# Optimization experiments

Measured on AMD Instinct MI355X. Metric: run time of the kernel, lower is better.

Reference implementation:

```python
import jax, jax.numpy as jnp
import numpy as np

N = 50000      # nodes
E = 800000     # edges (avg degree 16)
D = 128        # node_embedding_dim
H = 256        # hidden_dim


def setup_inputs() -> dict:
    key = jax.random.key(0)
    ks = jax.random.split(key, 12)
    init = lambda k, shape, fan: (jax.random.normal(k, shape, jnp.float32) / np.sqrt(fan).astype(np.float32))
    return {
        "node_ids": jnp.arange(N, dtype=jnp.int32),
        "edge_index": jax.random.randint(ks[0], (2, E), 0, N, jnp.int32),
        "neighbour_edge_index": jax.random.randint(ks[1], (2, E), 0, N, jnp.int32),
        "edge_attr": jax.random.uniform(ks[2], (E,), jnp.float32),
        "emb": init(ks[3], (N, D), D),          # Embedding table
        "W_in": init(ks[4], (D, H), D), "b_in": jnp.zeros((H,), jnp.float32),
        "W_out": init(ks[5], (H, D), H), "b_out": jnp.zeros((D,), jnp.float32),
        "W1": init(ks[6], (2 * D, D), 2 * D), "b1": jnp.zeros((D,), jnp.float32),
        "W2": init(ks[7], (D, D), D), "b2": jnp.zeros((D,), jnp.float32),
        "W3": init(ks[8], (D, 1), D), "b3": jnp.zeros((1,), jnp.float32),
    }


def gcn_conv(x, W, b, edge_index, w):
    """PyG GCNConv, add_self_loops=False, normalize=True.
    out_i = b + sum_{(j->i)} d_i^{-1/2} w_ji d_j^{-1/2} (x_j @ W)
    deg_i = sum of incoming edge weights at target node i.
    """
    row, col = edge_index[0], edge_index[1]
    deg = jax.ops.segment_sum(w, col, num_segments=N)
    dinv = jnp.where(deg > 0, 1.0 / jnp.sqrt(deg), 0.0)
    norm = dinv[row] * w * dinv[col]                    # [E]
    h = x @ W                                           # [N, out]
    msg = h[row] * norm[:, None]                        # [E, out]
    return jax.ops.segment_sum(msg, col, num_segments=N) + b


def reference(node_ids, edge_index, neighbour_edge_index, edge_attr,
              emb, W_in, b_in, W_out, b_out, W1, b1, W2, b2, W3, b3):
    x = emb[node_ids]                                   # embedding lookup [N, D]
    x = jax.nn.elu(gcn_conv(x, W_in, b_in, edge_index, edge_attr))
    ones = jnp.ones((neighbour_edge_index.shape[1],), x.dtype)
    x = jax.nn.elu(gcn_conv(x, W_out, b_out, neighbour_edge_index, ones))
    # edge-level gather-concat-MLP decoder
    src, dst = edge_index[0], edge_index[1]
    h = jnp.concatenate([x[src], x[dst]], axis=1)       # [E, 2D]
    h = jax.nn.relu(h @ W1 + b1)
    h = jax.nn.relu(h @ W2 + b2)
    return (h @ W3 + b3).squeeze(-1)                    # [E]
```

## Files before the change

### kernel.cpp

```cpp
#include <hip/hip_runtime.h>
#include <math.h>

#define NN 50000
#define NE 800000

typedef __attribute__((ext_vector_type(8))) short s8_t;
typedef __attribute__((ext_vector_type(4))) float f4_t;

__device__ __forceinline__ short bf16_rne(float v) {
  unsigned u = __float_as_uint(v);
  unsigned r = (u + 0x7FFFu + ((u >> 16) & 1u)) >> 16;
  return (short)r;
}
__device__ __forceinline__ float bf16_tof(short h) {
  return __uint_as_float(((unsigned)(unsigned short)h) << 16);
}
__device__ __forceinline__ void split2(float v, short& hi, short& lo) {
  hi = bf16_rne(v);
  lo = bf16_rne(v - bf16_tof(hi));
}


__global__ __launch_bounds__(256) void k_wcvt(const float* __restrict__ W1,
                                              const float* __restrict__ W2,
                                              const float* __restrict__ W_in,
                                              const float* __restrict__ W_out,
                                              short* __restrict__ w1th,
                                              short* __restrict__ w1tl,
                                              short* __restrict__ w2th,
                                              short* __restrict__ w2tl,
                                              short* __restrict__ winth,
                                              short* __restrict__ wintl,
                                              short* __restrict__ woutth,
                                              short* __restrict__ wouttl) {
  int i = blockIdx.x * 256 + threadIdx.x;
  if (i < 32768) {
    int k = i >> 7, n = i & 127;
    short h, l; split2(W1[i], h, l);
    w1th[n * 256 + k] = h; w1tl[n * 256 + k] = l;
  } else if (i < 49152) {
    int j = i - 32768;
    int k = j >> 7, n = j & 127;
    short h, l; split2(W2[j], h, l);
    w2th[n * 128 + k] = h; w2tl[n * 128 + k] = l;
  } else if (i < 81920) {
    int j = i - 49152;
    int k = j >> 8, n = j & 255;
    short h, l; split2(W_in[j], h, l);
    winth[n * 128 + k] = h; wintl[n * 128 + k] = l;
  } else if (i < 114688) {
    int j = i - 81920;
    int k = j >> 7, n = j & 127;
    short h, l; split2(W_out[j], h, l);
    woutth[n * 256 + k] = h; wouttl[n * 256 + k] = l;
  }
}


__global__ __launch_bounds__(256) void k_hist(const int* __restrict__ ei,
                                              const int* __restrict__ nei,
                                              const float* __restrict__ w,
                                              int* __restrict__ cnt1,
                                              float* __restrict__ deg1,
                                              int* __restrict__ cnt2) {
  int e = blockIdx.x * 256 + threadIdx.x;
  if (e < NE) {
    int c1 = ei[NE + e];
    atomicAdd(&cnt1[c1], 1);
    atomicAdd(&deg1[c1], w[e]);
    atomicAdd(&cnt2[nei[NE + e]], 1);
  }
}

__global__ __launch_bounds__(256) void k_dinvs(const float* __restrict__ deg1,
                                               const int* __restrict__ cnt2,
                                               float* __restrict__ dinv1,
                                               float* __restrict__ dinv2) {
  int i = blockIdx.x * 256 + threadIdx.x;
  if (i < NN) {
    float d1 = deg1[i];
    dinv1[i] = d1 > 0.f ? (1.0f / sqrtf(d1)) : 0.f;
    int c2 = cnt2[i];
    dinv2[i] = c2 > 0 ? (1.0f / sqrtf((float)c2)) : 0.f;
  }
}


#define NCHUNK 196

__global__ __launch_bounds__(256) void k_scan_part(const int* __restrict__ cnt1,
                                                   const int* __restrict__ cnt2,
                                                   int* __restrict__ part) {
  int g = blockIdx.x >= NCHUNK;
  int chunk = g ? blockIdx.x - NCHUNK : blockIdx.x;
  const int* cnt = g ? cnt2 : cnt1;
  int i = chunk * 256 + threadIdx.x;
  int v = (i < NN) ? cnt[i] : 0;
  __shared__ int sd[4];
#pragma unroll
  for (int o = 32; o; o >>= 1) v += __shfl_down(v, o);
  if ((threadIdx.x & 63) == 0) sd[threadIdx.x >> 6] = v;
  __syncthreads();
  if (threadIdx.x == 0) part[blockIdx.x] = sd[0] + sd[1] + sd[2] + sd[3];
}

__global__ __launch_bounds__(256) void k_scan_mid(int* __restrict__ part,
                                                  int* __restrict__ off1_last,
                                                  int* __restrict__ off2_last) {
  __shared__ int sd[256];
  for (int g = 0; g < 2; g++) {
    int base = g * NCHUNK;
    int v = (threadIdx.x < NCHUNK) ? part[base + threadIdx.x] : 0;
    sd[threadIdx.x] = v;
    __syncthreads();
    for (int o = 1; o < 256; o <<= 1) {
      int x = (threadIdx.x >= o) ? sd[threadIdx.x - o] : 0;
      __syncthreads();
      sd[threadIdx.x] += x;
      __syncthreads();
    }
    if (threadIdx.x < NCHUNK) part[base + threadIdx.x] = sd[threadIdx.x] - v;
    if (threadIdx.x == 255) *(g ? off2_last : off1_last) = sd[255];
    __syncthreads();
  }
}

__global__ __launch_bounds__(256) void k_scan_final(const int* __restrict__ cnt1,
                                                    const int* __restrict__ cnt2,
                                                    const int* __restrict__ part,
                                                    int* __restrict__ off1,
                                                    int* __restrict__ pos1,
                                                    int* __restrict__ off2,
                                                    int* __restrict__ pos2) {
  int g = blockIdx.x >= NCHUNK;
  int chunk = g ? blockIdx.x - NCHUNK : blockIdx.x;
  const int* cnt = g ? cnt2 : cnt1;
  int* off = g ? off2 : off1;
  int* pos = g ? pos2 : pos1;
  __shared__ int sd[256];
  int i = chunk * 256 + threadIdx.x;
  int v = (i < NN) ? cnt[i] : 0;
  sd[threadIdx.x] = v;
  __syncthreads();
  for (int o = 1; o < 256; o <<= 1) {
    int x = (threadIdx.x >= o) ? sd[threadIdx.x - o] : 0;
    __syncthreads();
    sd[threadIdx.x] += x;
    __syncthreads();
  }
  if (i < NN) {
    int ex = part[blockIdx.x] + sd[threadIdx.x] - v;
    off[i] = ex; pos[i] = ex;
  }
}


__global__ __launch_bounds__(256) void k_fill(const int* __restrict__ ei,
                                              const int* __restrict__ nei,
                                              const float* __restrict__ w,
                                              const float* __restrict__ dinv1,
                                              const float* __restrict__ dinv2,
                                              int* __restrict__ pos1,
                                              int4* __restrict__ c1pack,
                                              int* __restrict__ pos2,
                                              int2* __restrict__ c2pack) {
  int e = blockIdx.x * 256 + threadIdx.x;
  if (e < NE) {
    int r = ei[e], c = ei[NE + e];
    float nv = dinv1[r] * w[e] * dinv1[c];
    int s = atomicAdd(&pos1[c], 1);
    c1pack[s] = make_int4(r, c, e, __float_as_int(nv));
    int r2 = nei[e], c2v = nei[NE + e];
    float nv2 = dinv2[r2] * dinv2[c2v];
    int s2 = atomicAdd(&pos2[c2v], 1);
    c2pack[s2] = make_int2(r2, __float_as_int(nv2));
  }
}


__global__ __launch_bounds__(256) void k_agg1(const int* __restrict__ off,
                                              const int4* __restrict__ c1pack,
                                              const int* __restrict__ ids,
                                              const float* __restrict__ emb,
                                              short* __restrict__ aggXh,
                                              short* __restrict__ aggXl) {
  int wave = threadIdx.x >> 6, lane = threadIdx.x & 63;
  int h = lane >> 5, sub = lane & 31;
  int node = blockIdx.x * 4 + wave;
  int start = off[node], end = off[node + 1];
  float4 acc = make_float4(0.f, 0.f, 0.f, 0.f);
  int i = start + h;
  for (; i + 14 < end; i += 16) {
    float4 v[8]; float n[8];
#pragma unroll
    for (int k = 0; k < 8; k++) {
      int4 p = c1pack[i + 2 * k];
      n[k] = __int_as_float(p.w);
      v[k] = *(const float4*)(emb + (size_t)ids[p.x] * 128 + sub * 4);
    }
#pragma unroll
    for (int k = 0; k < 8; k++) {
      acc.x = fmaf(n[k], v[k].x, acc.x);
      acc.y = fmaf(n[k], v[k].y, acc.y);
      acc.z = fmaf(n[k], v[k].z, acc.z);
      acc.w = fmaf(n[k], v[k].w, acc.w);
    }
  }
  for (; i < end; i += 2) {
    int4 p = c1pack[i];
    float n0 = __int_as_float(p.w);
    float4 v0 = *(const float4*)(emb + (size_t)ids[p.x] * 128 + sub * 4);
    acc.x = fmaf(n0, v0.x, acc.x);
    acc.y = fmaf(n0, v0.y, acc.y);
    acc.z = fmaf(n0, v0.z, acc.z);
    acc.w = fmaf(n0, v0.w, acc.w);
  }
  acc.x += __shfl_xor(acc.x, 32);
  acc.y += __shfl_xor(acc.y, 32);
  acc.z += __shfl_xor(acc.z, 32);
  acc.w += __shfl_xor(acc.w, 32);
  if (h == 0) {
    short h0, l0, h1, l1, h2, l2, h3, l3;
    split2(acc.x, h0, l0); split2(acc.y, h1, l1);
    split2(acc.z, h2, l2); split2(acc.w, h3, l3);
    uint2 hp, lp;
    hp.x = (unsigned)(unsigned short)h0 | ((unsigned)(unsigned short)h1 << 16);
    hp.y = (unsigned)(unsigned short)h2 | ((unsigned)(unsigned short)h3 << 16);
    lp.x = (unsigned)(unsigned short)l0 | ((unsigned)(unsigned short)l1 << 16);
    lp.y = (unsigned)(unsigned short)l2 | ((unsigned)(unsigned short)l3 << 16);
    *(uint2*)(aggXh + (size_t)node * 128 + sub * 4) = hp;
    *(uint2*)(aggXl + (size_t)node * 128 + sub * 4) = lp;
  }
}


__global__ __launch_bounds__(256) void k_agg2(const int* __restrict__ off,
                                              const int2* __restrict__ c2pack,
                                              const float* __restrict__ h2,
                                              const float* __restrict__ b,
                                              short* __restrict__ xh,
                                              short* __restrict__ xl) {
  int wave = threadIdx.x >> 6, lane = threadIdx.x & 63;
  int h = lane >> 5, sub = lane & 31;
  int node = blockIdx.x * 4 + wave;
  int start = off[node], end = off[node + 1];
  float4 acc = make_float4(0.f, 0.f, 0.f, 0.f);
  int i = start + h;
  for (; i + 14 < end; i += 16) {
    float4 v[8]; float n[8];
#pragma unroll
    for (int k = 0; k < 8; k++) {
      int2 p = c2pack[i + 2 * k];
      n[k] = __int_as_float(p.y);
      v[k] = *(const float4*)(h2 + (size_t)p.x * 128 + sub * 4);
    }
#pragma unroll
    for (int k = 0; k < 8; k++) {
      acc.x = fmaf(n[k], v[k].x, acc.x);
      acc.y = fmaf(n[k], v[k].y, acc.y);
      acc.z = fmaf(n[k], v[k].z, acc.z);
      acc.w = fmaf(n[k], v[k].w, acc.w);
    }
  }
  for (; i < end; i += 2) {
    int2 p = c2pack[i];
    float n0 = __int_as_float(p.y);
    float4 v0 = *(const float4*)(h2 + (size_t)p.x * 128 + sub * 4);
    acc.x = fmaf(n0, v0.x, acc.x);
    acc.y = fmaf(n0, v0.y, acc.y);
    acc.z = fmaf(n0, v0.z, acc.z);
    acc.w = fmaf(n0, v0.w, acc.w);
  }
  acc.x += __shfl_xor(acc.x, 32);
  acc.y += __shfl_xor(acc.y, 32);
  acc.z += __shfl_xor(acc.z, 32);
  acc.w += __shfl_xor(acc.w, 32);
  if (h == 0) {
    float4 bb = *(const float4*)(b + sub * 4);
    float v0 = acc.x + bb.x, v1 = acc.y + bb.y;
    float v2 = acc.z + bb.z, v3 = acc.w + bb.w;
    v0 = v0 > 0.f ? v0 : expm1f(v0);
    v1 = v1 > 0.f ? v1 : expm1f(v1);
    v2 = v2 > 0.f ? v2 : expm1f(v2);
    v3 = v3 > 0.f ? v3 : expm1f(v3);
    short h0, l0, h1, l1, h2s, l2, h3, l3;
    split2(v0, h0, l0); split2(v1, h1, l1);
    split2(v2, h2s, l2); split2(v3, h3, l3);
    uint2 hp, lp;
    hp.x = (unsigned)(unsigned short)h0 | ((unsigned)(unsigned short)h1 << 16);
    hp.y = (unsigned)(unsigned short)h2s | ((unsigned)(unsigned short)h3 << 16);
    lp.x = (unsigned)(unsigned short)l0 | ((unsigned)(unsigned short)l1 << 16);
    lp.y = (unsigned)(unsigned short)l2 | ((unsigned)(unsigned short)l3 << 16);
    *(uint2*)(xh + (size_t)node * 128 + sub * 4) = hp;
    *(uint2*)(xl + (size_t)node * 128 + sub * 4) = lp;
  }
}


__global__ __launch_bounds__(256) void k_gemm1m(const short* __restrict__ aggXh,
                                                const short* __restrict__ aggXl,
                                                const short* __restrict__ winth,
                                                const short* __restrict__ wintl,
                                                const float* __restrict__ b,
                                                short* __restrict__ x1h,
                                                short* __restrict__ x1l) {
  __shared__ short Xh[32 * 136];
  __shared__ short Xl[32 * 136];
  int t = threadIdx.x;
  int n0 = blockIdx.x * 32;
#pragma unroll
  for (int j = 0; j < 2; j++) {
    int i = t + 256 * j;
    int row = i >> 4, q = i & 15;
    int node = n0 + row; if (node >= NN) node = NN - 1;
    *(uint4*)&Xh[row * 136 + q * 8] = *(const uint4*)(aggXh + (size_t)node * 128 + q * 8);
    *(uint4*)&Xl[row * 136 + q * 8] = *(const uint4*)(aggXl + (size_t)node * 128 + q * 8);
  }
  __syncthreads();

  int w = t >> 6, lane = t & 63;
  int quad = lane >> 4, l16 = lane & 15;
  int nb = w * 64;
  int aoff0 = l16 * 136 + quad * 8;
  int aoff1 = (16 + l16) * 136 + quad * 8;

  f4_t acc[2][4];
#pragma unroll
  for (int mi = 0; mi < 2; mi++)
#pragma unroll
    for (int ni = 0; ni < 4; ni++) acc[mi][ni] = (f4_t){0.f, 0.f, 0.f, 0.f};

#pragma unroll
  for (int kb = 0; kb < 4; kb++) {
    int k0 = kb * 32;
    s8_t ah0 = *(const s8_t*)&Xh[aoff0 + k0];
    s8_t ah1 = *(const s8_t*)&Xh[aoff1 + k0];
    s8_t al0 = *(const s8_t*)&Xl[aoff0 + k0];
    s8_t al1 = *(const s8_t*)&Xl[aoff1 + k0];
#pragma unroll
    for (int ni = 0; ni < 4; ni++) {
      int bo = (nb + ni * 16 + l16) * 128 + quad * 8 + k0;
      s8_t bh = *(const s8_t*)(winth + bo);
      s8_t bl = *(const s8_t*)(wintl + bo);
      acc[0][ni] = __builtin_amdgcn_mfma_f32_16x16x32_bf16(ah0, bh, acc[0][ni], 0, 0, 0);
      acc[0][ni] = __builtin_amdgcn_mfma_f32_16x16x32_bf16(ah0, bl, acc[0][ni], 0, 0, 0);
      acc[0][ni] = __builtin_amdgcn_mfma_f32_16x16x32_bf16(al0, bh, acc[0][ni], 0, 0, 0);
      acc[1][ni] = __builtin_amdgcn_mfma_f32_16x16x32_bf16(ah1, bh, acc[1][ni], 0, 0, 0);
      acc[1][ni] = __builtin_amdgcn_mfma_f32_16x16x32_bf16(ah1, bl, acc[1][ni], 0, 0, 0);
      acc[1][ni] = __builtin_amdgcn_mfma_f32_16x16x32_bf16(al1, bh, acc[1][ni], 0, 0, 0);
    }
  }

#pragma unroll
  for (int mi = 0; mi < 2; mi++)
#pragma unroll
    for (int ni = 0; ni < 4; ni++) {
      int col = nb + ni * 16 + l16;
      float bv = b[col];
#pragma unroll
      for (int r = 0; r < 4; r++) {
        int node = n0 + mi * 16 + quad * 4 + r;
        if (node < NN) {
          float v = acc[mi][ni][r] + bv;
          v = v > 0.f ? v : expm1f(v);
          short hh, ll; split2(v, hh, ll);
          x1h[(size_t)node * 256 + col] = hh;
          x1l[(size_t)node * 256 + col] = ll;
        }
      }
    }
}


__global__ __launch_bounds__(256) void k_gemm2m(const short* __restrict__ x1h,
                                                const short* __restrict__ x1l,
                                                const short* __restrict__ woutth,
                                                const short* __restrict__ wouttl,
                                                float* __restrict__ h2) {
  __shared__ short Xh[32 * 264];
  __shared__ short Xl[32 * 264];
  int t = threadIdx.x;
  int n0 = blockIdx.x * 32;
#pragma unroll
  for (int j = 0; j < 4; j++) {
    int i = t + 256 * j;
    int row = i >> 5, q = i & 31;
    int node = n0 + row; if (node >= NN) node = NN - 1;
    *(uint4*)&Xh[row * 264 + q * 8] = *(const uint4*)(x1h + (size_t)node * 256 + q * 8);
    *(uint4*)&Xl[row * 264 + q * 8] = *(const uint4*)(x1l + (size_t)node * 256 + q * 8);
  }
  __syncthreads();

  int w = t >> 6, lane = t & 63;
  int quad = lane >> 4, l16 = lane & 15;
  int nb = w * 32;
  int aoff0 = l16 * 264 + quad * 8;
  int aoff1 = (16 + l16) * 264 + quad * 8;

  f4_t acc[2][2];
#pragma unroll
  for (int mi = 0; mi < 2; mi++)
#pragma unroll
    for (int ni = 0; ni < 2; ni++) acc[mi][ni] = (f4_t){0.f, 0.f, 0.f, 0.f};

#pragma unroll
  for (int kb = 0; kb < 8; kb++) {
    int k0 = kb * 32;
    s8_t ah0 = *(const s8_t*)&Xh[aoff0 + k0];
    s8_t ah1 = *(const s8_t*)&Xh[aoff1 + k0];
    s8_t al0 = *(const s8_t*)&Xl[aoff0 + k0];
    s8_t al1 = *(const s8_t*)&Xl[aoff1 + k0];
#pragma unroll
    for (int ni = 0; ni < 2; ni++) {
      int bo = (nb + ni * 16 + l16) * 256 + quad * 8 + k0;
      s8_t bh = *(const s8_t*)(woutth + bo);
      s8_t bl = *(const s8_t*)(wouttl + bo);
      acc[0][ni] = __builtin_amdgcn_mfma_f32_16x16x32_bf16(ah0, bh, acc[0][ni], 0, 0, 0);
      acc[0][ni] = __builtin_amdgcn_mfma_f32_16x16x32_bf16(ah0, bl, acc[0][ni], 0, 0, 0);
      acc[0][ni] = __builtin_amdgcn_mfma_f32_16x16x32_bf16(al0, bh, acc[0][ni], 0, 0, 0);
      acc[1][ni] = __builtin_amdgcn_mfma_f32_16x16x32_bf16(ah1, bh, acc[1][ni], 0, 0, 0);
      acc[1][ni] = __builtin_amdgcn_mfma_f32_16x16x32_bf16(ah1, bl, acc[1][ni], 0, 0, 0);
      acc[1][ni] = __builtin_amdgcn_mfma_f32_16x16x32_bf16(al1, bh, acc[1][ni], 0, 0, 0);
    }
  }

#pragma unroll
  for (int mi = 0; mi < 2; mi++)
#pragma unroll
    for (int ni = 0; ni < 2; ni++) {
      int col = nb + ni * 16 + l16;
#pragma unroll
      for (int r = 0; r < 4; r++) {
        int node = n0 + mi * 16 + quad * 4 + r;
        if (node < NN) h2[(size_t)node * 128 + col] = acc[mi][ni][r];
      }
    }
}


__global__ __launch_bounds__(256) void k_pab(const short* __restrict__ x2h,
                                             const short* __restrict__ x2l,
                                             const short* __restrict__ w1th,
                                             const short* __restrict__ w1tl,
                                             const float* __restrict__ b1,
                                             float* __restrict__ Pa,
                                             float* __restrict__ Pb) {
  __shared__ short Xh[32 * 136];
  __shared__ short Xl[32 * 136];
  int t = threadIdx.x;
  int n0 = blockIdx.x * 32;
#pragma unroll
  for (int j = 0; j < 2; j++) {
    int i = t + 256 * j;
    int row = i >> 4, q = i & 15;
    int node = n0 + row; if (node >= NN) node = NN - 1;
    *(uint4*)&Xh[row * 136 + q * 8] = *(const uint4*)(x2h + (size_t)node * 128 + q * 8);
    *(uint4*)&Xl[row * 136 + q * 8] = *(const uint4*)(x2l + (size_t)node * 128 + q * 8);
  }
  __syncthreads();

  int w = t >> 6, lane = t & 63;
  int quad = lane >> 4, l16 = lane & 15;
  int nb = w * 32;
  int aoff0 = l16 * 136 + quad * 8;
  int aoff1 = (16 + l16) * 136 + quad * 8;
  int bo0 = (nb + l16) * 256 + quad * 8;
  int bo1 = (nb + 16 + l16) * 256 + quad * 8;

  f4_t aa[2][2], ab[2][2];
#pragma unroll
  for (int mi = 0; mi < 2; mi++)
#pragma unroll
    for (int ni = 0; ni < 2; ni++) {
      aa[mi][ni] = (f4_t){0.f, 0.f, 0.f, 0.f};
      ab[mi][ni] = (f4_t){0.f, 0.f, 0.f, 0.f};
    }

#pragma unroll
  for (int kb = 0; kb < 4; kb++) {
    int k0 = kb * 32;
    s8_t ah0 = *(const s8_t*)&Xh[aoff0 + k0];
    s8_t ah1 = *(const s8_t*)&Xh[aoff1 + k0];
    s8_t al0 = *(const s8_t*)&Xl[aoff0 + k0];
    s8_t al1 = *(const s8_t*)&Xl[aoff1 + k0];
    {
      s8_t bh0 = *(const s8_t*)(w1th + bo0 + k0);
      s8_t bh1 = *(const s8_t*)(w1th + bo1 + k0);
      s8_t bl0 = *(const s8_t*)(w1tl + bo0 + k0);
      s8_t bl1 = *(const s8_t*)(w1tl + bo1 + k0);
      aa[0][0] = __builtin_amdgcn_mfma_f32_16x16x32_bf16(ah0, bh0, aa[0][0], 0, 0, 0);
      aa[0][0] = __builtin_amdgcn_mfma_f32_16x16x32_bf16(ah0, bl0, aa[0][0], 0, 0, 0);
      aa[0][0] = __builtin_amdgcn_mfma_f32_16x16x32_bf16(al0, bh0, aa[0][0], 0, 0, 0);
      aa[0][1] = __builtin_amdgcn_mfma_f32_16x16x32_bf16(ah0, bh1, aa[0][1], 0, 0, 0);
      aa[0][1] = __builtin_amdgcn_mfma_f32_16x16x32_bf16(ah0, bl1, aa[0][1], 0, 0, 0);
      aa[0][1] = __builtin_amdgcn_mfma_f32_16x16x32_bf16(al0, bh1, aa[0][1], 0, 0, 0);
      aa[1][0] = __builtin_amdgcn_mfma_f32_16x16x32_bf16(ah1, bh0, aa[1][0], 0, 0, 0);
      aa[1][0] = __builtin_amdgcn_mfma_f32_16x16x32_bf16(ah1, bl0, aa[1][0], 0, 0, 0);
      aa[1][0] = __builtin_amdgcn_mfma_f32_16x16x32_bf16(al1, bh0, aa[1][0], 0, 0, 0);
      aa[1][1] = __builtin_amdgcn_mfma_f32_16x16x32_bf16(ah1, bh1, aa[1][1], 0, 0, 0);
      aa[1][1] = __builtin_amdgcn_mfma_f32_16x16x32_bf16(ah1, bl1, aa[1][1], 0, 0, 0);
      aa[1][1] = __builtin_amdgcn_mfma_f32_16x16x32_bf16(al1, bh1, aa[1][1], 0, 0, 0);
    }
    {
      s8_t bh0 = *(const s8_t*)(w1th + bo0 + 128 + k0);
      s8_t bh1 = *(const s8_t*)(w1th + bo1 + 128 + k0);
      s8_t bl0 = *(const s8_t*)(w1tl + bo0 + 128 + k0);
      s8_t bl1 = *(const s8_t*)(w1tl + bo1 + 128 + k0);
      ab[0][0] = __builtin_amdgcn_mfma_f32_16x16x32_bf16(ah0, bh0, ab[0][0], 0, 0, 0);
      ab[0][0] = __builtin_amdgcn_mfma_f32_16x16x32_bf16(ah0, bl0, ab[0][0], 0, 0, 0);
      ab[0][0] = __builtin_amdgcn_mfma_f32_16x16x32_bf16(al0, bh0, ab[0][0], 0, 0, 0);
      ab[0][1] = __builtin_amdgcn_mfma_f32_16x16x32_bf16(ah0, bh1, ab[0][1], 0, 0, 0);
      ab[0][1] = __builtin_amdgcn_mfma_f32_16x16x32_bf16(ah0, bl1, ab[0][1], 0, 0, 0);
      ab[0][1] = __builtin_amdgcn_mfma_f32_16x16x32_bf16(al0, bh1, ab[0][1], 0, 0, 0);
      ab[1][0] = __builtin_amdgcn_mfma_f32_16x16x32_bf16(ah1, bh0, ab[1][0], 0, 0, 0);
      ab[1][0] = __builtin_amdgcn_mfma_f32_16x16x32_bf16(ah1, bl0, ab[1][0], 0, 0, 0);
      ab[1][0] = __builtin_amdgcn_mfma_f32_16x16x32_bf16(al1, bh0, ab[1][0], 0, 0, 0);
      ab[1][1] = __builtin_amdgcn_mfma_f32_16x16x32_bf16(ah1, bh1, ab[1][1], 0, 0, 0);
      ab[1][1] = __builtin_amdgcn_mfma_f32_16x16x32_bf16(ah1, bl1, ab[1][1], 0, 0, 0);
      ab[1][1] = __builtin_amdgcn_mfma_f32_16x16x32_bf16(al1, bh1, ab[1][1], 0, 0, 0);
    }
  }

  float b1v0 = b1[nb + l16], b1v1 = b1[nb + 16 + l16];
#pragma unroll
  for (int mi = 0; mi < 2; mi++)
#pragma unroll
    for (int ni = 0; ni < 2; ni++) {
      int col = nb + ni * 16 + l16;
      float bv = ni ? b1v1 : b1v0;
#pragma unroll
      for (int r = 0; r < 4; r++) {
        int node = n0 + mi * 16 + quad * 4 + r;
        if (node < NN) {
          Pa[(size_t)node * 128 + col] = aa[mi][ni][r];
          Pb[(size_t)node * 128 + col] = ab[mi][ni][r] + bv;
        }
      }
    }
}


#define ST 136

__global__ __launch_bounds__(256, 4) void k_decoder(
    const float* __restrict__ Pa, const float* __restrict__ Pb,
    const int4* __restrict__ c1pack,
    const short* __restrict__ w2th, const short* __restrict__ w2tl,
    const float* __restrict__ b2,
    const float* __restrict__ W3, const float* __restrict__ b3,
    float* __restrict__ out) {
  __shared__ short Th[32 * ST];
  __shared__ short Tl[32 * ST];
  __shared__ float part[4][32];

  int t = threadIdx.x;
  int b = blockIdx.x;
  int id = (b & 7) * 3125 + (b >> 3);
  int s0base = id * 32;

#pragma unroll
  for (int j = 0; j < 2; j++) {
    int i = t + 256 * j;
    int le = i >> 4, q = i & 15;
    int4 p = c1pack[s0base + le];
    const float* pa = Pa + (size_t)p.x * 128 + q * 8;
    const float* pb = Pb + (size_t)p.y * 128 + q * 8;
    float4 a0 = *(const float4*)(pa);
    float4 a1 = *(const float4*)(pa + 4);
    float4 c0 = *(const float4*)(pb);
    float4 c1 = *(const float4*)(pb + 4);
    float v[8];
    v[0] = a0.x + c0.x; v[1] = a0.y + c0.y;
    v[2] = a0.z + c0.z; v[3] = a0.w + c0.w;
    v[4] = a1.x + c1.x; v[5] = a1.y + c1.y;
    v[6] = a1.z + c1.z; v[7] = a1.w + c1.w;
    s8_t hv, lv;
#pragma unroll
    for (int k = 0; k < 8; k++) {
      float x = fmaxf(v[k], 0.f);
      short h, l; split2(x, h, l);
      hv[k] = h; lv[k] = l;
    }
    *(s8_t*)&Th[le * ST + q * 8] = hv;
    *(s8_t*)&Tl[le * ST + q * 8] = lv;
  }
  __syncthreads();

  int w = t >> 6, lane = t & 63;
  int quad = lane >> 4, l16 = lane & 15;
  int nb = w * 32;
  float b2v0 = b2[nb + l16], b2v1 = b2[nb + 16 + l16];
  float w3a = W3[nb + l16], w3b = W3[nb + 16 + l16];

  int toff0 = l16 * ST + quad * 8;
  int toff1 = (16 + l16) * ST + quad * 8;
  int coff0 = (nb + l16) * 128 + quad * 8;
  int coff1 = (nb + 16 + l16) * 128 + quad * 8;

  f4_t acc2[2][2];
#pragma unroll
  for (int mi = 0; mi < 2; mi++)
#pragma unroll
    for (int ni = 0; ni < 2; ni++) acc2[mi][ni] = (f4_t){0.f, 0.f, 0.f, 0.f};

#pragma unroll
  for (int kb = 0; kb < 4; kb++) {
    int k0 = kb * 32;
    s8_t ah0 = *(const s8_t*)&Th[toff0 + k0];
    s8_t ah1 = *(const s8_t*)&Th[toff1 + k0];
    s8_t al0 = *(const s8_t*)&Tl[toff0 + k0];
    s8_t al1 = *(const s8_t*)&Tl[toff1 + k0];
    s8_t bh0 = *(const s8_t*)(w2th + coff0 + k0);
    s8_t bh1 = *(const s8_t*)(w2th + coff1 + k0);
    s8_t bl0 = *(const s8_t*)(w2tl + coff0 + k0);
    s8_t bl1 = *(const s8_t*)(w2tl + coff1 + k0);
    acc2[0][0] = __builtin_amdgcn_mfma_f32_16x16x32_bf16(ah0, bh0, acc2[0][0], 0, 0, 0);
    acc2[0][0] = __builtin_amdgcn_mfma_f32_16x16x32_bf16(ah0, bl0, acc2[0][0], 0, 0, 0);
    acc2[0][0] = __builtin_amdgcn_mfma_f32_16x16x32_bf16(al0, bh0, acc2[0][0], 0, 0, 0);
    acc2[0][1] = __builtin_amdgcn_mfma_f32_16x16x32_bf16(ah0, bh1, acc2[0][1], 0, 0, 0);
    acc2[0][1] = __builtin_amdgcn_mfma_f32_16x16x32_bf16(ah0, bl1, acc2[0][1], 0, 0, 0);
    acc2[0][1] = __builtin_amdgcn_mfma_f32_16x16x32_bf16(al0, bh1, acc2[0][1], 0, 0, 0);
    acc2[1][0] = __builtin_amdgcn_mfma_f32_16x16x32_bf16(ah1, bh0, acc2[1][0], 0, 0, 0);
    acc2[1][0] = __builtin_amdgcn_mfma_f32_16x16x32_bf16(ah1, bl0, acc2[1][0], 0, 0, 0);
    acc2[1][0] = __builtin_amdgcn_mfma_f32_16x16x32_bf16(al1, bh0, acc2[1][0], 0, 0, 0);
    acc2[1][1] = __builtin_amdgcn_mfma_f32_16x16x32_bf16(ah1, bh1, acc2[1][1], 0, 0, 0);
    acc2[1][1] = __builtin_amdgcn_mfma_f32_16x16x32_bf16(ah1, bl1, acc2[1][1], 0, 0, 0);
    acc2[1][1] = __builtin_amdgcn_mfma_f32_16x16x32_bf16(al1, bh1, acc2[1][1], 0, 0, 0);
  }

#pragma unroll
  for (int mi = 0; mi < 2; mi++) {
#pragma unroll
    for (int r = 0; r < 4; r++) {
      float pv = fmaxf(acc2[mi][0][r] + b2v0, 0.f) * w3a +
                 fmaxf(acc2[mi][1][r] + b2v1, 0.f) * w3b;
      pv += __shfl_xor(pv, 1);
      pv += __shfl_xor(pv, 2);
      pv += __shfl_xor(pv, 4);
      pv += __shfl_xor(pv, 8);
      if (l16 == 0) part[w][mi * 16 + quad * 4 + r] = pv;
    }
  }
  __syncthreads();

  if (t < 32) {
    float s = part[0][t] + part[1][t] + part[2][t] + part[3][t] + b3[0];
    int4 p = c1pack[s0base + t];
    out[p.z] = s;
  }
}


extern "C" void kernel_launch(void* const* d_in, const int* in_sizes, int n_in,
                              void* d_out, int out_size, void* d_ws, size_t ws_size,
                              hipStream_t stream) {
  const int*   node_ids = (const int*)d_in[0];
  const int*   ei       = (const int*)d_in[1];
  const int*   nei      = (const int*)d_in[2];
  const float* eattr    = (const float*)d_in[3];
  const float* emb      = (const float*)d_in[4];
  const float* W_in     = (const float*)d_in[5];
  const float* b_in     = (const float*)d_in[6];
  const float* W_out    = (const float*)d_in[7];
  const float* b_out    = (const float*)d_in[8];
  const float* W1       = (const float*)d_in[9];
  const float* b1       = (const float*)d_in[10];
  const float* W2       = (const float*)d_in[11];
  const float* b2       = (const float*)d_in[12];
  const float* W3       = (const float*)d_in[13];
  const float* b3       = (const float*)d_in[14];
  float* out = (float*)d_out;

  float* ws    = (float*)d_ws;
  float* bufA  = ws;
  float* bufB  = bufA + (size_t)NN * 128;
  int*   cnt1  = (int*)(bufB + (size_t)NN * 256);
  int*   cnt2  = cnt1 + NN;
  float* deg1  = (float*)(cnt2 + NN);
  float* dinv1 = deg1 + NN;
  float* dinv2 = dinv1 + NN;
  int*   off1  = (int*)(dinv2 + NN);
  int*   pos1  = off1 + NN + 1;
  int*   off2  = pos1 + NN;
  int*   pos2  = off2 + NN + 1;
  int4*  c1pack = (int4*)((((uintptr_t)(pos2 + NN)) + 15) & ~(uintptr_t)15);
  int2*  c2pack = (int2*)(c1pack + NE);
  short* w1th   = (short*)(c2pack + NE);
  short* w1tl   = w1th + 32768;
  short* w2th   = w1tl + 32768;
  short* w2tl   = w2th + 16384;
  short* winth  = w2tl + 16384;
  short* wintl  = winth + 32768;
  short* woutth = wintl + 32768;
  short* wouttl = woutth + 32768;
  int*   part   = (int*)(wouttl + 32768);

  short* aggXh = (short*)bufA;
  short* aggXl = aggXh + (size_t)NN * 128;
  float* h2    = bufA;
  float* Pa    = bufA;
  short* x1h   = (short*)bufB;
  short* x1l   = x1h + (size_t)NN * 256;
  short* x2h   = (short*)bufB;
  short* x2l   = x2h + (size_t)NN * 128;
  float* Pb    = bufB + (size_t)NN * 128;

  k_wcvt<<<448, 256, 0, stream>>>(W1, W2, W_in, W_out,
                                  w1th, w1tl, w2th, w2tl,
                                  winth, wintl, woutth, wouttl);

  hipMemsetAsync(cnt1, 0, 3 * (size_t)NN * sizeof(int), stream);
  k_hist<<<NE / 256, 256, 0, stream>>>(ei, nei, eattr, cnt1, deg1, cnt2);
  k_dinvs<<<(NN + 255) / 256, 256, 0, stream>>>(deg1, cnt2, dinv1, dinv2);
  k_scan_part<<<2 * NCHUNK, 256, 0, stream>>>(cnt1, cnt2, part);
  k_scan_mid<<<1, 256, 0, stream>>>(part, off1 + NN, off2 + NN);
  k_scan_final<<<2 * NCHUNK, 256, 0, stream>>>(cnt1, cnt2, part,
                                               off1, pos1, off2, pos2);
  k_fill<<<NE / 256, 256, 0, stream>>>(ei, nei, eattr, dinv1, dinv2,
                                       pos1, c1pack, pos2, c2pack);

  k_agg1<<<NN / 4, 256, 0, stream>>>(off1, c1pack, node_ids, emb, aggXh, aggXl);
  k_gemm1m<<<(NN + 31) / 32, 256, 0, stream>>>(aggXh, aggXl, winth, wintl,
                                               b_in, x1h, x1l);

  k_gemm2m<<<(NN + 31) / 32, 256, 0, stream>>>(x1h, x1l, woutth, wouttl, h2);
  k_agg2<<<NN / 4, 256, 0, stream>>>(off2, c2pack, h2, b_out, x2h, x2l);

  k_pab<<<(NN + 31) / 32, 256, 0, stream>>>(x2h, x2l, w1th, w1tl, b1, Pa, Pb);

  k_decoder<<<NE / 32, 256, 0, stream>>>(Pa, Pb, c1pack,
                                         w2th, w2tl, b2, W3, b3, out);
}
```

Baseline: 760.7 us.

## Fuse neighbour aggregation into following GEMM kernels and merge dinv into scan

After: 797.9 us. +4.9%, slower.

```diff
diff --git a/kernel.cpp b/kernel.cpp
--- a/kernel.cpp
+++ b/kernel.cpp
@@ -72,34 +72,33 @@
   }
 }
 
-__global__ __launch_bounds__(256) void k_dinvs(const float* __restrict__ deg1,
-                                               const int* __restrict__ cnt2,
-                                               float* __restrict__ dinv1,
-                                               float* __restrict__ dinv2) {
-  int i = blockIdx.x * 256 + threadIdx.x;
-  if (i < NN) {
-    float d1 = deg1[i];
-    dinv1[i] = d1 > 0.f ? (1.0f / sqrtf(d1)) : 0.f;
-    int c2 = cnt2[i];
-    dinv2[i] = c2 > 0 ? (1.0f / sqrtf((float)c2)) : 0.f;
-  }
-}
-
 
 #define NCHUNK 196
 
 __global__ __launch_bounds__(256) void k_scan_part(const int* __restrict__ cnt1,
                                                    const int* __restrict__ cnt2,
+                                                   const float* __restrict__ deg1,
+                                                   float* __restrict__ dinv1,
+                                                   float* __restrict__ dinv2,
                                                    int* __restrict__ part) {
   int g = blockIdx.x >= NCHUNK;
   int chunk = g ? blockIdx.x - NCHUNK : blockIdx.x;
   const int* cnt = g ? cnt2 : cnt1;
   int i = chunk * 256 + threadIdx.x;
   int v = (i < NN) ? cnt[i] : 0;
+  if (i < NN) {
+    if (!g) {
+      float d1 = deg1[i];
+      dinv1[i] = d1 > 0.f ? (1.0f / sqrtf(d1)) : 0.f;
+    } else {
+      dinv2[i] = v > 0 ? (1.0f / sqrtf((float)v)) : 0.f;
+    }
+  }
   __shared__ int sd[4];
-#pragma unroll
-  for (int o = 32; o; o >>= 1) v += __shfl_down(v, o);
-  if ((threadIdx.x & 63) == 0) sd[threadIdx.x >> 6] = v;
+  int r = v;
+#pragma unroll
+  for (int o = 32; o; o >>= 1) r += __shfl_down(r, o);
+  if ((threadIdx.x & 63) == 0) sd[threadIdx.x >> 6] = r;
   __syncthreads();
   if (threadIdx.x == 0) part[blockIdx.x] = sd[0] + sd[1] + sd[2] + sd[3];
 }
@@ -178,147 +177,77 @@
 }
 
 
-__global__ __launch_bounds__(256) void k_agg1(const int* __restrict__ off,
-                                              const int4* __restrict__ c1pack,
-                                              const int* __restrict__ ids,
-                                              const float* __restrict__ emb,
-                                              short* __restrict__ aggXh,
-                                              short* __restrict__ aggXl) {
-  int wave = threadIdx.x >> 6, lane = threadIdx.x & 63;
-  int h = lane >> 5, sub = lane & 31;
-  int node = blockIdx.x * 4 + wave;
-  int start = off[node], end = off[node + 1];
-  float4 acc = make_float4(0.f, 0.f, 0.f, 0.f);
-  int i = start + h;
-  for (; i + 14 < end; i += 16) {
-    float4 v[8]; float n[8];
-#pragma unroll
-    for (int k = 0; k < 8; k++) {
-      int4 p = c1pack[i + 2 * k];
-      n[k] = __int_as_float(p.w);
-      v[k] = *(const float4*)(emb + (size_t)ids[p.x] * 128 + sub * 4);
-    }
-#pragma unroll
-    for (int k = 0; k < 8; k++) {
-      acc.x = fmaf(n[k], v[k].x, acc.x);
-      acc.y = fmaf(n[k], v[k].y, acc.y);
-      acc.z = fmaf(n[k], v[k].z, acc.z);
-      acc.w = fmaf(n[k], v[k].w, acc.w);
-    }
-  }
-  for (; i < end; i += 2) {
-    int4 p = c1pack[i];
-    float n0 = __int_as_float(p.w);
-    float4 v0 = *(const float4*)(emb + (size_t)ids[p.x] * 128 + sub * 4);
-    acc.x = fmaf(n0, v0.x, acc.x);
-    acc.y = fmaf(n0, v0.y, acc.y);
-    acc.z = fmaf(n0, v0.z, acc.z);
-    acc.w = fmaf(n0, v0.w, acc.w);
-  }
-  acc.x += __shfl_xor(acc.x, 32);
-  acc.y += __shfl_xor(acc.y, 32);
-  acc.z += __shfl_xor(acc.z, 32);
-  acc.w += __shfl_xor(acc.w, 32);
-  if (h == 0) {
-    short h0, l0, h1, l1, h2, l2, h3, l3;
-    split2(acc.x, h0, l0); split2(acc.y, h1, l1);
-    split2(acc.z, h2, l2); split2(acc.w, h3, l3);
-    uint2 hp, lp;
-    hp.x = (unsigned)(unsigned short)h0 | ((unsigned)(unsigned short)h1 << 16);
-    hp.y = (unsigned)(unsigned short)h2 | ((unsigned)(unsigned short)h3 << 16);
-    lp.x = (unsigned)(unsigned short)l0 | ((unsigned)(unsigned short)l1 << 16);
-    lp.y = (unsigned)(unsigned short)l2 | ((unsigned)(unsigned short)l3 << 16);
-    *(uint2*)(aggXh + (size_t)node * 128 + sub * 4) = hp;
-    *(uint2*)(aggXl + (size_t)node * 128 + sub * 4) = lp;
-  }
-}
-
-
-__global__ __launch_bounds__(256) void k_agg2(const int* __restrict__ off,
-                                              const int2* __restrict__ c2pack,
-                                              const float* __restrict__ h2,
-                                              const float* __restrict__ b,
-                                              short* __restrict__ xh,
-                                              short* __restrict__ xl) {
-  int wave = threadIdx.x >> 6, lane = threadIdx.x & 63;
-  int h = lane >> 5, sub = lane & 31;
-  int node = blockIdx.x * 4 + wave;
-  int start = off[node], end = off[node + 1];
-  float4 acc = make_float4(0.f, 0.f, 0.f, 0.f);
-  int i = start + h;
-  for (; i + 14 < end; i += 16) {
-    float4 v[8]; float n[8];
-#pragma unroll
-    for (int k = 0; k < 8; k++) {
-      int2 p = c2pack[i + 2 * k];
-      n[k] = __int_as_float(p.y);
-      v[k] = *(const float4*)(h2 + (size_t)p.x * 128 + sub * 4);
-    }
-#pragma unroll
-    for (int k = 0; k < 8; k++) {
-      acc.x = fmaf(n[k], v[k].x, acc.x);
-      acc.y = fmaf(n[k], v[k].y, acc.y);
-      acc.z = fmaf(n[k], v[k].z, acc.z);
-      acc.w = fmaf(n[k], v[k].w, acc.w);
-    }
-  }
-  for (; i < end; i += 2) {
-    int2 p = c2pack[i];
-    float n0 = __int_as_float(p.y);
-    float4 v0 = *(const float4*)(h2 + (size_t)p.x * 128 + sub * 4);
-    acc.x = fmaf(n0, v0.x, acc.x);
-    acc.y = fmaf(n0, v0.y, acc.y);
-    acc.z = fmaf(n0, v0.z, acc.z);
-    acc.w = fmaf(n0, v0.w, acc.w);
-  }
-  acc.x += __shfl_xor(acc.x, 32);
-  acc.y += __shfl_xor(acc.y, 32);
-  acc.z += __shfl_xor(acc.z, 32);
-  acc.w += __shfl_xor(acc.w, 32);
-  if (h == 0) {
-    float4 bb = *(const float4*)(b + sub * 4);
-    float v0 = acc.x + bb.x, v1 = acc.y + bb.y;
-    float v2 = acc.z + bb.z, v3 = acc.w + bb.w;
-    v0 = v0 > 0.f ? v0 : expm1f(v0);
-    v1 = v1 > 0.f ? v1 : expm1f(v1);
-    v2 = v2 > 0.f ? v2 : expm1f(v2);
-    v3 = v3 > 0.f ? v3 : expm1f(v3);
-    short h0, l0, h1, l1, h2s, l2, h3, l3;
-    split2(v0, h0, l0); split2(v1, h1, l1);
-    split2(v2, h2s, l2); split2(v3, h3, l3);
-    uint2 hp, lp;
-    hp.x = (unsigned)(unsigned short)h0 | ((unsigned)(unsigned short)h1 << 16);
-    hp.y = (unsigned)(unsigned short)h2s | ((unsigned)(unsigned short)h3 << 16);
-    lp.x = (unsigned)(unsigned short)l0 | ((unsigned)(unsigned short)l1 << 16);
-    lp.y = (unsigned)(unsigned short)l2 | ((unsigned)(unsigned short)l3 << 16);
-    *(uint2*)(xh + (size_t)node * 128 + sub * 4) = hp;
-    *(uint2*)(xl + (size_t)node * 128 + sub * 4) = lp;
-  }
-}
-
-
-__global__ __launch_bounds__(256) void k_gemm1m(const short* __restrict__ aggXh,
-                                                const short* __restrict__ aggXl,
-                                                const short* __restrict__ winth,
-                                                const short* __restrict__ wintl,
-                                                const float* __restrict__ b,
-                                                short* __restrict__ x1h,
-                                                short* __restrict__ x1l) {
+__global__ __launch_bounds__(256) void k_l1a(const int* __restrict__ off,
+                                             const int4* __restrict__ c1pack,
+                                             const int* __restrict__ ids,
+                                             const float* __restrict__ emb,
+                                             const short* __restrict__ winth,
+                                             const short* __restrict__ wintl,
+                                             const float* __restrict__ b,
+                                             short* __restrict__ x1h,
+                                             short* __restrict__ x1l) {
   __shared__ short Xh[32 * 136];
   __shared__ short Xl[32 * 136];
   int t = threadIdx.x;
+  int wave = t >> 6, lane = t & 63;
+  int h = lane >> 5, sub = lane & 31;
   int n0 = blockIdx.x * 32;
-#pragma unroll
-  for (int j = 0; j < 2; j++) {
-    int i = t + 256 * j;
-    int row = i >> 4, q = i & 15;
-    int node = n0 + row; if (node >= NN) node = NN - 1;
-    *(uint4*)&Xh[row * 136 + q * 8] = *(const uint4*)(aggXh + (size_t)node * 128 + q * 8);
-    *(uint4*)&Xl[row * 136 + q * 8] = *(const uint4*)(aggXl + (size_t)node * 128 + q * 8);
+
+  for (int kk = 0; kk < 8; kk++) {
+    int row = wave * 8 + kk;
+    int node = n0 + row;
+    float4 acc = make_float4(0.f, 0.f, 0.f, 0.f);
+    if (node < NN) {
+      int start = off[node], end = off[node + 1];
+      int i = start + h;
+      for (; i + 14 < end; i += 16) {
+        float4 v[8]; float n[8];
+#pragma unroll
+        for (int k = 0; k < 8; k++) {
+          int4 p = c1pack[i + 2 * k];
+          n[k] = __int_as_float(p.w);
+          v[k] = *(const float4*)(emb + (size_t)ids[p.x] * 128 + sub * 4);
+        }
+#pragma unroll
+        for (int k = 0; k < 8; k++) {
+          acc.x = fmaf(n[k], v[k].x, acc.x);
+          acc.y = fmaf(n[k], v[k].y, acc.y);
+          acc.z = fmaf(n[k], v[k].z, acc.z);
+          acc.w = fmaf(n[k], v[k].w, acc.w);
+        }
+      }
+      for (; i < end; i += 2) {
+        int4 p = c1pack[i];
+        float n0v = __int_as_float(p.w);
+        float4 v0 = *(const float4*)(emb + (size_t)ids[p.x] * 128 + sub * 4);
+        acc.x = fmaf(n0v, v0.x, acc.x);
+        acc.y = fmaf(n0v, v0.y, acc.y);
+        acc.z = fmaf(n0v, v0.z, acc.z);
+        acc.w = fmaf(n0v, v0.w, acc.w);
+      }
+    }
+    acc.x += __shfl_xor(acc.x, 32);
+    acc.y += __shfl_xor(acc.y, 32);
+    acc.z += __shfl_xor(acc.z, 32);
+    acc.w += __shfl_xor(acc.w, 32);
+    if (h == 0) {
+      uint2 hp = make_uint2(0u, 0u), lp = make_uint2(0u, 0u);
+      if (node < NN) {
+        short h0, l0, h1, l1, h2, l2, h3, l3;
+        split2(acc.x, h0, l0); split2(acc.y, h1, l1);
+        split2(acc.z, h2, l2); split2(acc.w, h3, l3);
+        hp.x = (unsigned)(unsigned short)h0 | ((unsigned)(unsigned short)h1 << 16);
+        hp.y = (unsigned)(unsigned short)h2 | ((unsigned)(unsigned short)h3 << 16);
+        lp.x = (unsigned)(unsigned short)l0 | ((unsigned)(unsigned short)l1 << 16);
+        lp.y = (unsigned)(unsigned short)l2 | ((unsigned)(unsigned short)l3 << 16);
+      }
+      *(uint2*)&Xh[row * 136 + sub * 4] = hp;
+      *(uint2*)&Xl[row * 136 + sub * 4] = lp;
+    }
   }
   __syncthreads();
 
-  int w = t >> 6, lane = t & 63;
+  int w = wave;
   int quad = lane >> 4, l16 = lane & 15;
   int nb = w * 64;
   int aoff0 = l16 * 136 + quad * 8;
@@ -438,8 +367,10 @@
 }
 
 
-__global__ __launch_bounds__(256) void k_pab(const short* __restrict__ x2h,
-                                             const short* __restrict__ x2l,
+__global__ __launch_bounds__(256) void k_l2b(const int* __restrict__ off,
+                                             const int2* __restrict__ c2pack,
+                                             const float* __restrict__ h2,
+                                             const float* __restrict__ b,
                                              const short* __restrict__ w1th,
                                              const short* __restrict__ w1tl,
                                              const float* __restrict__ b1,
@@ -448,18 +379,72 @@
   __shared__ short Xh[32 * 136];
   __shared__ short Xl[32 * 136];
   int t = threadIdx.x;
+  int wave = t >> 6, lane = t & 63;
+  int h = lane >> 5, sub = lane & 31;
   int n0 = blockIdx.x * 32;
-#pragma unroll
-  for (int j = 0; j < 2; j++) {
-    int i = t + 256 * j;
-    int row = i >> 4, q = i & 15;
-    int node = n0 + row; if (node >= NN) node = NN - 1;
-    *(uint4*)&Xh[row * 136 + q * 8] = *(const uint4*)(x2h + (size_t)node * 128 + q * 8);
-    *(uint4*)&Xl[row * 136 + q * 8] = *(const uint4*)(x2l + (size_t)node * 128 + q * 8);
+
+  for (int kk = 0; kk < 8; kk++) {
+    int row = wave * 8 + kk;
+    int node = n0 + row;
+    float4 acc = make_float4(0.f, 0.f, 0.f, 0.f);
+    if (node < NN) {
+      int start = off[node], end = off[node + 1];
+      int i = start + h;
+      for (; i + 14 < end; i += 16) {
+        float4 v[8]; float n[8];
+#pragma unroll
+        for (int k = 0; k < 8; k++) {
+          int2 p = c2pack[i + 2 * k];
+          n[k] = __int_as_float(p.y);
+          v[k] = *(const float4*)(h2 + (size_t)p.x * 128 + sub * 4);
+        }
+#pragma unroll
+        for (int k = 0; k < 8; k++) {
+          acc.x = fmaf(n[k], v[k].x, acc.x);
+          acc.y = fmaf(n[k], v[k].y, acc.y);
+          acc.z = fmaf(n[k], v[k].z, acc.z);
+          acc.w = fmaf(n[k], v[k].w, acc.w);
+        }
+      }
+      for (; i < end; i += 2) {
+        int2 p = c2pack[i];
+        float n0v = __int_as_float(p.y);
+        float4 v0 = *(const float4*)(h2 + (size_t)p.x * 128 + sub * 4);
+        acc.x = fmaf(n0v, v0.x, acc.x);
+        acc.y = fmaf(n0v, v0.y, acc.y);
+        acc.z = fmaf(n0v, v0.z, acc.z);
+        acc.w = fmaf(n0v, v0.w, acc.w);
+      }
+    }
+    acc.x += __shfl_xor(acc.x, 32);
+    acc.y += __shfl_xor(acc.y, 32);
+    acc.z += __shfl_xor(acc.z, 32);
+    acc.w += __shfl_xor(acc.w, 32);
+    if (h == 0) {
+      uint2 hp = make_uint2(0u, 0u), lp = make_uint2(0u, 0u);
+      if (node < NN) {
+        float4 bb = *(const float4*)(b + sub * 4);
+        float v0 = acc.x + bb.x, v1 = acc.y + bb.y;
+        float v2 = acc.z + bb.z, v3 = acc.w + bb.w;
+        v0 = v0 > 0.f ? v0 : expm1f(v0);
+        v1 = v1 > 0.f ? v1 : expm1f(v1);
+        v2 = v2 > 0.f ? v2 : expm1f(v2);
+        v3 = v3 > 0.f ? v3 : expm1f(v3);
+        short h0, l0, h1, l1, h2s, l2, h3, l3;
+        split2(v0, h0, l0); split2(v1, h1, l1);
+        split2(v2, h2s, l2); split2(v3, h3, l3);
+        hp.x = (unsigned)(unsigned short)h0 | ((unsigned)(unsigned short)h1 << 16);
+        hp.y = (unsigned)(unsigned short)h2s | ((unsigned)(unsigned short)h3 << 16);
+        lp.x = (unsigned)(unsigned short)l0 | ((unsigned)(unsigned short)l1 << 16);
+        lp.y = (unsigned)(unsigned short)l2 | ((unsigned)(unsigned short)l3 << 16);
+      }
+      *(uint2*)&Xh[row * 136 + sub * 4] = hp;
+      *(uint2*)&Xl[row * 136 + sub * 4] = lp;
+    }
   }
   __syncthreads();
 
-  int w = t >> 6, lane = t & 63;
+  int w = wave;
   int quad = lane >> 4, l16 = lane & 15;
   int nb = w * 32;
   int aoff0 = l16 * 136 + quad * 8;
@@ -558,31 +543,46 @@
   int id = (b & 7) * 3125 + (b >> 3);
   int s0base = id * 32;
 
-#pragma unroll
-  for (int j = 0; j < 2; j++) {
-    int i = t + 256 * j;
-    int le = i >> 4, q = i & 15;
-    int4 p = c1pack[s0base + le];
-    const float* pa = Pa + (size_t)p.x * 128 + q * 8;
-    const float* pb = Pb + (size_t)p.y * 128 + q * 8;
-    float4 a0 = *(const float4*)(pa);
-    float4 a1 = *(const float4*)(pa + 4);
-    float4 c0 = *(const float4*)(pb);
-    float4 c1 = *(const float4*)(pb + 4);
-    float v[8];
-    v[0] = a0.x + c0.x; v[1] = a0.y + c0.y;
-    v[2] = a0.z + c0.z; v[3] = a0.w + c0.w;
-    v[4] = a1.x + c1.x; v[5] = a1.y + c1.y;
-    v[6] = a1.z + c1.z; v[7] = a1.w + c1.w;
-    s8_t hv, lv;
+  {
+    int le0 = t >> 4, q = t & 15;
+    int4 p0 = c1pack[s0base + le0];
+    int4 p1 = c1pack[s0base + le0 + 16];
+    const float* pa0 = Pa + (size_t)p0.x * 128 + q * 8;
+    const float* pb0 = Pb + (size_t)p0.y * 128 + q * 8;
+    const float* pa1 = Pa + (size_t)p1.x * 128 + q * 8;
+    const float* pb1 = Pb + (size_t)p1.y * 128 + q * 8;
+    float4 ra0 = *(const float4*)(pa0);
+    float4 ra1 = *(const float4*)(pa0 + 4);
+    float4 rb0 = *(const float4*)(pb0);
+    float4 rb1 = *(const float4*)(pb0 + 4);
+    float4 ra2 = *(const float4*)(pa1);
+    float4 ra3 = *(const float4*)(pa1 + 4);
+    float4 rb2 = *(const float4*)(pb1);
+    float4 rb3 = *(const float4*)(pb1 + 4);
+
+    float v0[8], v1[8];
+    v0[0] = ra0.x + rb0.x; v0[1] = ra0.y + rb0.y;
+    v0[2] = ra0.z + rb0.z; v0[3] = ra0.w + rb0.w;
+    v0[4] = ra1.x + rb1.x; v0[5] = ra1.y + rb1.y;
+    v0[6] = ra1.z + rb1.z; v0[7] = ra1.w + rb1.w;
+    v1[0] = ra2.x + rb2.x; v1[1] = ra2.y + rb2.y;
+    v1[2] = ra2.z + rb2.z; v1[3] = ra2.w + rb2.w;
+    v1[4] = ra3.x + rb3.x; v1[5] = ra3.y + rb3.y;
+    v1[6] = ra3.z + rb3.z; v1[7] = ra3.w + rb3.w;
+
+    s8_t hv0, lv0, hv1, lv1;
 #pragma unroll
     for (int k = 0; k < 8; k++) {
-      float x = fmaxf(v[k], 0.f);
-      short h, l; split2(x, h, l);
-      hv[k] = h; lv[k] = l;
-    }
-    *(s8_t*)&Th[le * ST + q * 8] = hv;
-    *(s8_t*)&Tl[le * ST + q * 8] = lv;
+      float x0 = fmaxf(v0[k], 0.f);
+      float x1 = fmaxf(v1[k], 0.f);
+      short hh, ll;
+      split2(x0, hh, ll); hv0[k] = hh; lv0[k] = ll;
+      split2(x1, hh, ll); hv1[k] = hh; lv1[k] = ll;
+    }
+    *(s8_t*)&Th[le0 * ST + q * 8] = hv0;
+    *(s8_t*)&Tl[le0 * ST + q * 8] = lv0;
+    *(s8_t*)&Th[(le0 + 16) * ST + q * 8] = hv1;
+    *(s8_t*)&Tl[(le0 + 16) * ST + q * 8] = lv1;
   }
   __syncthreads();
 
@@ -695,14 +695,10 @@
   short* wouttl = woutth + 32768;
   int*   part   = (int*)(wouttl + 32768);
 
-  short* aggXh = (short*)bufA;
-  short* aggXl = aggXh + (size_t)NN * 128;
   float* h2    = bufA;
-  float* Pa    = bufA;
   short* x1h   = (short*)bufB;
   short* x1l   = x1h + (size_t)NN * 256;
-  short* x2h   = (short*)bufB;
-  short* x2l   = x2h + (size_t)NN * 128;
+  float* Pa    = bufB;
   float* Pb    = bufB + (size_t)NN * 128;
 
   k_wcvt<<<448, 256, 0, stream>>>(W1, W2, W_in, W_out,
@@ -711,22 +707,20 @@
 
   hipMemsetAsync(cnt1, 0, 3 * (size_t)NN * sizeof(int), stream);
   k_hist<<<NE / 256, 256, 0, stream>>>(ei, nei, eattr, cnt1, deg1, cnt2);
-  k_dinvs<<<(NN + 255) / 256, 256, 0, stream>>>(deg1, cnt2, dinv1, dinv2);
-  k_scan_part<<<2 * NCHUNK, 256, 0, stream>>>(cnt1, cnt2, part);
+  k_scan_part<<<2 * NCHUNK, 256, 0, stream>>>(cnt1, cnt2, deg1, dinv1, dinv2, part);
   k_scan_mid<<<1, 256, 0, stream>>>(part, off1 + NN, off2 + NN);
   k_scan_final<<<2 * NCHUNK, 256, 0, stream>>>(cnt1, cnt2, part,
                                                off1, pos1, off2, pos2);
   k_fill<<<NE / 256, 256, 0, stream>>>(ei, nei, eattr, dinv1, dinv2,
                                        pos1, c1pack, pos2, c2pack);
 
-  k_agg1<<<NN / 4, 256, 0, stream>>>(off1, c1pack, node_ids, emb, aggXh, aggXl);
-  k_gemm1m<<<(NN + 31) / 32, 256, 0, stream>>>(aggXh, aggXl, winth, wintl,
-                                               b_in, x1h, x1l);
+  k_l1a<<<(NN + 31) / 32, 256, 0, stream>>>(off1, c1pack, node_ids, emb,
+                                            winth, wintl, b_in, x1h, x1l);
 
   k_gemm2m<<<(NN + 31) / 32, 256, 0, stream>>>(x1h, x1l, woutth, wouttl, h2);
-  k_agg2<<<NN / 4, 256, 0, stream>>>(off2, c2pack, h2, b_out, x2h, x2l);
-
-  k_pab<<<(NN + 31) / 32, 256, 0, stream>>>(x2h, x2l, w1th, w1tl, b1, Pa, Pb);
+
+  k_l2b<<<(NN + 31) / 32, 256, 0, stream>>>(off2, c2pack, h2, b_out,
+                                            w1th, w1tl, b1, Pa, Pb);
 
   k_decoder<<<NE / 32, 256, 0, stream>>>(Pa, Pb, c1pack,
                                          w2th, w2tl, b2, W3, b3, out);
```
